# Optimization experiments

Hardware: AMD Instinct MI355X
Metric: run time of the kernel (lower is better)

Reference implementation:

```python
import jax, jax.numpy as jnp
import numpy as np

COMMITMENT_COST = 0.25


def setup_inputs() -> dict:
    key = jax.random.key(0)
    k1, k2 = jax.random.split(key)
    B, K, D = 1048576, 16, 64
    z = jax.random.normal(k1, (B, D), dtype=jnp.float32)
    # nn.Embedding init: uniform(-1/K, 1/K)
    embedding = jax.random.uniform(k2, (K, D), dtype=jnp.float32,
                                   minval=-1.0 / K, maxval=1.0 / K)
    return {"z": z, "embedding": embedding}


def reference(z, embedding):
    # squared L2 distances: ||z||^2 + ||e||^2 - 2 z e^T  -> [B, K]
    distances = (jnp.sum(z * z, axis=1, keepdims=True)
                 + jnp.sum(embedding * embedding, axis=1)
                 - 2.0 * jnp.matmul(z, embedding.T))
    encoding_indices = jnp.argmin(distances, axis=1)           # [B]
    quantized = embedding[encoding_indices]                    # [B, D]

    commitment_loss = jnp.mean((z - jax.lax.stop_gradient(quantized)) ** 2)
    embedding_loss = jnp.mean((jax.lax.stop_gradient(z) - quantized) ** 2)
    vq_loss = embedding_loss + COMMITMENT_COST * commitment_loss

    # straight-through estimator
    quantized = z + jax.lax.stop_gradient(quantized - z)
    return quantized, encoding_indices, vq_loss
```

## Files before the change

### kernel.cpp

```cpp
#include <hip/hip_runtime.h>

#define B_ROWS 1048576
#define K_CODES 16
#define D_DIM 64

constexpr int BLOCK = 256;
constexpr int GRID  = 2048;

__device__ __forceinline__ float xor1_dpp(float x) {
    return __builtin_bit_cast(float,
        __builtin_amdgcn_update_dpp(0, __builtin_bit_cast(int, x), 0xB1 ,
                                    0xF, 0xF, true));
}
__device__ __forceinline__ float xor2_dpp(float x) {
    return __builtin_bit_cast(float,
        __builtin_amdgcn_update_dpp(0, __builtin_bit_cast(int, x), 0x4E ,
                                    0xF, 0xF, true));
}
__device__ __forceinline__ float xor4_sw(float x) {
    return __builtin_bit_cast(float,
        __builtin_amdgcn_ds_swizzle(__builtin_bit_cast(int, x), 0x101F));
}
__device__ __forceinline__ float xor8_sw(float x) {
    return __builtin_bit_cast(float,
        __builtin_amdgcn_ds_swizzle(__builtin_bit_cast(int, x), 0x201F));
}

__global__ __launch_bounds__(BLOCK)
void vq_main(const float* __restrict__ z,
             const float* __restrict__ emb,
             float* __restrict__ out_q,
             float* __restrict__ out_idx,
             float* __restrict__ partials)
{
    __shared__ __align__(16) float s_emb[K_CODES * D_DIM];
    __shared__ float s_se[K_CODES];
    __shared__ float s_w[BLOCK / 64];

    const int t = threadIdx.x;

    ((float4*)s_emb)[t] = ((const float4*)emb)[t];
    __syncthreads();

    if (t < K_CODES) {
        float s = 0.f;
        #pragma unroll
        for (int c = 0; c < D_DIM; ++c) {
            float e = s_emb[t * D_DIM + c];
            s = fmaf(e, e, s);
        }
        s_se[t] = s;
    }
    __syncthreads();

    const int j = t & 15;
    float4 ereg[16];
    #pragma unroll
    for (int r = 0; r < 16; ++r)
        ereg[r] = *(const float4*)&s_emb[((r ^ j) * D_DIM) + j * 4];
    const float se_j = s_se[j];

    float lossacc = 0.f;

    const int gid    = (blockIdx.x * BLOCK + t) >> 4;
    const int stride = (GRID * BLOCK) >> 4;

    int row = gid;
    float4 zv = *(const float4*)&z[(size_t)row * D_DIM + j * 4];

    while (row < B_ROWS) {
        const int nrow = row + stride;
        float4 zn = zv;
        if (nrow < B_ROWS)
            zn = *(const float4*)&z[(size_t)nrow * D_DIM + j * 4];

        float p[16];
        #pragma unroll
        for (int r = 0; r < 16; ++r) {
            float4 e = ereg[r];
            p[r] = fmaf(zv.w, e.w, fmaf(zv.z, e.z, fmaf(zv.y, e.y, zv.x * e.x)));
        }

        float szp = fmaf(zv.w, zv.w, fmaf(zv.z, zv.z, fmaf(zv.y, zv.y, zv.x * zv.x)));
        szp += xor1_dpp(szp);
        szp += xor2_dpp(szp);
        szp += xor4_sw(szp);
        szp += xor8_sw(szp);

        #pragma unroll
        for (int r = 0; r < 16; r += 2)  p[r] += xor1_dpp(p[r + 1]);
        #pragma unroll
        for (int r = 0; r < 16; r += 4)  p[r] += xor2_dpp(p[r + 2]);
        #pragma unroll
        for (int r = 0; r < 16; r += 8)  p[r] += xor4_sw(p[r + 4]);
        p[0] += xor8_sw(p[8]);
        const float dot = p[0];

        const float d = (szp + se_j) - 2.0f * dot;

        float vmin = d;
        vmin = fminf(vmin, xor1_dpp(vmin));
        vmin = fminf(vmin, xor2_dpp(vmin));
        vmin = fminf(vmin, xor4_sw(vmin));
        vmin = fminf(vmin, xor8_sw(vmin));
        unsigned long long bal = __ballot(d == vmin);
        unsigned int mask = (unsigned int)((bal >> (t & 48)) & 0xFFFFull);
        int kmin = __ffs(mask) - 1;

        const float4 qv = *(const float4*)&s_emb[kmin * D_DIM + j * 4];

        float dx = zv.x - qv.x; lossacc = fmaf(dx, dx, lossacc);
        dx = zv.y - qv.y;       lossacc = fmaf(dx, dx, lossacc);
        dx = zv.z - qv.z;       lossacc = fmaf(dx, dx, lossacc);
        dx = zv.w - qv.w;       lossacc = fmaf(dx, dx, lossacc);

        *(float4*)&out_q[(size_t)row * D_DIM + j * 4] = qv;
        if (j == 0) out_idx[row] = (float)kmin;

        zv  = zn;
        row = nrow;
    }

    lossacc += __shfl_xor(lossacc, 32, 64);
    lossacc += __shfl_xor(lossacc, 16, 64);
    lossacc += __shfl_xor(lossacc, 8, 64);
    lossacc += __shfl_xor(lossacc, 4, 64);
    lossacc += __shfl_xor(lossacc, 2, 64);
    lossacc += __shfl_xor(lossacc, 1, 64);
    if ((t & 63) == 0) s_w[t >> 6] = lossacc;
    __syncthreads();
    if (t == 0) partials[blockIdx.x] = (s_w[0] + s_w[1]) + (s_w[2] + s_w[3]);
}

__global__ void vq_finalize(const float* __restrict__ partials, int n,
                            float* __restrict__ out_loss)
{
    __shared__ float sw[4];
    float s = 0.f;
    for (int i = threadIdx.x; i < n; i += 256) s += partials[i];
    s += __shfl_xor(s, 32, 64);
    s += __shfl_xor(s, 16, 64);
    s += __shfl_xor(s, 8, 64);
    s += __shfl_xor(s, 4, 64);
    s += __shfl_xor(s, 2, 64);
    s += __shfl_xor(s, 1, 64);
    if ((threadIdx.x & 63) == 0) sw[threadIdx.x >> 6] = s;
    __syncthreads();
    if (threadIdx.x == 0) {
        float tot = (sw[0] + sw[1]) + (sw[2] + sw[3]);
        *out_loss = tot * (1.25f / (float)(B_ROWS * (size_t)D_DIM));
    }
}

extern "C" void kernel_launch(void* const* d_in, const int* in_sizes, int n_in,
                              void* d_out, int out_size, void* d_ws, size_t ws_size,
                              hipStream_t stream)
{
    const float* z   = (const float*)d_in[0];
    const float* emb = (const float*)d_in[1];
    float* out      = (float*)d_out;
    float* out_q    = out;
    float* out_idx  = out + (size_t)B_ROWS * D_DIM;
    float* out_loss = out_idx + B_ROWS;
    float* partials = (float*)d_ws;

    vq_main<<<GRID, BLOCK, 0, stream>>>(z, emb, out_q, out_idx, partials);
    vq_finalize<<<1, 256, 0, stream>>>(partials, GRID, out_loss);
}
```

Before: 114.2 us.

## Replace ds_swizzle reductions with row-mirror DPP and add nontemporal loads/stores

Replaces the xor-4 and xor-8 lane exchanges, which used ds_swizzle (an LDS-path instruction), with DPP row_half_mirror and row_mirror permutations. This lets every reduction step run as cheap ALU-side DPP. To keep the results correct, lanes get a permuted column mapping (sj) so that the mirror patterns form a valid butterfly, and the partial-sum reduction tree is reordered to match. It also switches z loads and quantized-output stores to nontemporal hints to reduce cache pollution in this streaming kernel. The risk is that the remapped lane/column layout changes coalescing order and must stay consistent for the argmin to be correct.

```diff
diff --git a/kernel.cpp b/kernel.cpp
--- a/kernel.cpp
+++ b/kernel.cpp
@@ -7,23 +7,23 @@
 constexpr int BLOCK = 256;
 constexpr int GRID  = 2048;
 
+typedef float f32x4 __attribute__((ext_vector_type(4)));
+
 __device__ __forceinline__ float xor1_dpp(float x) {
     return __builtin_bit_cast(float,
-        __builtin_amdgcn_update_dpp(0, __builtin_bit_cast(int, x), 0xB1 ,
-                                    0xF, 0xF, true));
+        __builtin_amdgcn_update_dpp(0, __builtin_bit_cast(int, x), 0xB1, 0xF, 0xF, true));
 }
 __device__ __forceinline__ float xor2_dpp(float x) {
     return __builtin_bit_cast(float,
-        __builtin_amdgcn_update_dpp(0, __builtin_bit_cast(int, x), 0x4E ,
-                                    0xF, 0xF, true));
+        __builtin_amdgcn_update_dpp(0, __builtin_bit_cast(int, x), 0x4E, 0xF, 0xF, true));
 }
-__device__ __forceinline__ float xor4_sw(float x) {
+__device__ __forceinline__ float xor7_dpp(float x) {
     return __builtin_bit_cast(float,
-        __builtin_amdgcn_ds_swizzle(__builtin_bit_cast(int, x), 0x101F));
+        __builtin_amdgcn_update_dpp(0, __builtin_bit_cast(int, x), 0x141, 0xF, 0xF, true));
 }
-__device__ __forceinline__ float xor8_sw(float x) {
+__device__ __forceinline__ float xor15_dpp(float x) {
     return __builtin_bit_cast(float,
-        __builtin_amdgcn_ds_swizzle(__builtin_bit_cast(int, x), 0x201F));
+        __builtin_amdgcn_update_dpp(0, __builtin_bit_cast(int, x), 0x140, 0xF, 0xF, true));
 }
 
 __global__ __launch_bounds__(BLOCK)
@@ -54,10 +54,13 @@
     __syncthreads();
 
     const int j = t & 15;
+    const int sj = ((j & 1) ? 8 : 0) ^ ((j & 2) ? 4 : 0)
+                 ^ ((j & 4) ? 14 : 0) ^ ((j & 8) ? 3 : 0);
+
     float4 ereg[16];
     #pragma unroll
     for (int r = 0; r < 16; ++r)
-        ereg[r] = *(const float4*)&s_emb[((r ^ j) * D_DIM) + j * 4];
+        ereg[r] = *(const float4*)&s_emb[((r ^ j) * D_DIM) + sj * 4];
     const float se_j = s_se[j];
 
     float lossacc = 0.f;
@@ -66,13 +69,13 @@
     const int stride = (GRID * BLOCK) >> 4;
 
     int row = gid;
-    float4 zv = *(const float4*)&z[(size_t)row * D_DIM + j * 4];
+    f32x4 zv = __builtin_nontemporal_load((const f32x4*)&z[(size_t)row * D_DIM + sj * 4]);
 
     while (row < B_ROWS) {
         const int nrow = row + stride;
-        float4 zn = zv;
+        f32x4 zn = zv;
         if (nrow < B_ROWS)
-            zn = *(const float4*)&z[(size_t)nrow * D_DIM + j * 4];
+            zn = __builtin_nontemporal_load((const f32x4*)&z[(size_t)nrow * D_DIM + sj * 4]);
 
         float p[16];
         #pragma unroll
@@ -84,16 +87,16 @@
         float szp = fmaf(zv.w, zv.w, fmaf(zv.z, zv.z, fmaf(zv.y, zv.y, zv.x * zv.x)));
         szp += xor1_dpp(szp);
         szp += xor2_dpp(szp);
-        szp += xor4_sw(szp);
-        szp += xor8_sw(szp);
+        szp += xor7_dpp(szp);
+        szp += xor15_dpp(szp);
 
         #pragma unroll
-        for (int r = 0; r < 16; r += 2)  p[r] += xor1_dpp(p[r + 1]);
+        for (int r = 0; r < 8; ++r)  p[r] += xor15_dpp(p[15 - r]);
         #pragma unroll
-        for (int r = 0; r < 16; r += 4)  p[r] += xor2_dpp(p[r + 2]);
-        #pragma unroll
-        for (int r = 0; r < 16; r += 8)  p[r] += xor4_sw(p[r + 4]);
-        p[0] += xor8_sw(p[8]);
+        for (int r = 0; r < 4; ++r)  p[r] += xor7_dpp(p[7 - r]);
+        p[0] += xor2_dpp(p[2]);
+        p[1] += xor2_dpp(p[3]);
+        p[0] += xor1_dpp(p[1]);
         const float dot = p[0];
 
         const float d = (szp + se_j) - 2.0f * dot;
@@ -101,20 +104,21 @@
         float vmin = d;
         vmin = fminf(vmin, xor1_dpp(vmin));
         vmin = fminf(vmin, xor2_dpp(vmin));
-        vmin = fminf(vmin, xor4_sw(vmin));
-        vmin = fminf(vmin, xor8_sw(vmin));
+        vmin = fminf(vmin, xor7_dpp(vmin));
+        vmin = fminf(vmin, xor15_dpp(vmin));
         unsigned long long bal = __ballot(d == vmin);
         unsigned int mask = (unsigned int)((bal >> (t & 48)) & 0xFFFFull);
         int kmin = __ffs(mask) - 1;
 
-        const float4 qv = *(const float4*)&s_emb[kmin * D_DIM + j * 4];
+        const float4 qv = *(const float4*)&s_emb[kmin * D_DIM + sj * 4];
 
         float dx = zv.x - qv.x; lossacc = fmaf(dx, dx, lossacc);
         dx = zv.y - qv.y;       lossacc = fmaf(dx, dx, lossacc);
         dx = zv.z - qv.z;       lossacc = fmaf(dx, dx, lossacc);
         dx = zv.w - qv.w;       lossacc = fmaf(dx, dx, lossacc);
 
-        *(float4*)&out_q[(size_t)row * D_DIM + j * 4] = qv;
+        f32x4 qn = { qv.x, qv.y, qv.z, qv.w };
+        __builtin_nontemporal_store(qn, (f32x4*)&out_q[(size_t)row * D_DIM + sj * 4]);
         if (j == 0) out_idx[row] = (float)kmin;
 
         zv  = zn;
```

Measured after the change: 107.7 us. 1.06x faster.
